# Kernel optimization log

Hardware: AMD Instinct MI355X
Metric: run time of the kernel (lower is better)

The kernel has to match this reference:

```python
import jax, jax.numpy as jnp
from jax import lax
import numpy as np

B, C_IN, C_OUT, H, W = 4, 256, 256, 4, 8192
HD = C_OUT // H          # head_dim = 64
K_ATT = 7
PAD = (1 * (K_ATT - 1) + 1) // 2  # = 3 (dilation=1)
CK = 1                   # conv_kernel_size (must be 1 for the module's shapes to be consistent)


def setup_inputs() -> dict:
    key = jax.random.key(0)
    ks = jax.random.split(key, 14)
    s = 0.05
    inp = {
        "x": jax.random.normal(ks[0], (B, C_IN, W), dtype=jnp.float32),
        # 1x1 convs q/k/v: weight [C_out, C_in], bias [C_out]
        "w1": jax.random.normal(ks[1], (C_OUT, C_IN), dtype=jnp.float32) * (C_IN ** -0.5),
        "b1": jax.random.normal(ks[2], (C_OUT,), dtype=jnp.float32) * s,
        "w2": jax.random.normal(ks[3], (C_OUT, C_IN), dtype=jnp.float32) * (C_IN ** -0.5),
        "b2": jax.random.normal(ks[4], (C_OUT,), dtype=jnp.float32) * s,
        "w3": jax.random.normal(ks[5], (C_OUT, C_IN), dtype=jnp.float32) * (C_IN ** -0.5),
        "b3": jax.random.normal(ks[6], (C_OUT,), dtype=jnp.float32) * s,
        # conv_p: Conv1d(1, head_dim, 1): weight [HD], bias [HD]
        "wp": jax.random.normal(ks[7], (HD,), dtype=jnp.float32) * s,
        "bp": jax.random.normal(ks[8], (HD,), dtype=jnp.float32) * s,
        # fc: Conv2d(3*H, CK, 1, bias=False): weight [CK, 3H]
        "fc_w": jax.random.normal(ks[9], (CK, 3 * H), dtype=jnp.float32) * ((3 * H) ** -0.5),
        # dep_conv: Conv1d(CK*HD -> C_OUT, kernel=CK, groups=HD): weight [C_OUT, CK, CK], bias [C_OUT]
        "dep_w": jax.random.normal(ks[10], (C_OUT, CK, CK), dtype=jnp.float32) * s,
        "dep_b": jax.random.normal(ks[11], (C_OUT,), dtype=jnp.float32) * s,
        "rate1": jnp.float32(0.5),
        "rate2": jnp.float32(0.5),
    }
    return inp


def _conv1x1(x, w, b):  # x: [B, Cin, W] -> [B, Cout, W]
    return jnp.einsum('oc,bcw->bow', w, x) + b[None, :, None]


def _unfold(p):  # p: [..., Wp] -> windows [..., W, K_ATT]
    idx = jnp.arange(W)[:, None] + jnp.arange(K_ATT)[None, :]
    return p[..., idx]


def _forward(x, w1, b1, w2, b2, w3, b3, wp, bp, fc_w, dep_w, dep_b, rate1, rate2):
    q = _conv1x1(x, w1, b1)   # [B, C, W]
    k = _conv1x1(x, w2, b2)
    v = _conv1x1(x, w3, b3)
    scaling = HD ** -0.5

    # positional encoding: conv_p(linspace(-1,1,W)) -> [HD, W]
    loc = jnp.linspace(-1.0, 1.0, W, dtype=jnp.float32)
    pe = wp[:, None] * loc[None, :] + bp[:, None]

    q_att = q.reshape(B * H, HD, W) * scaling
    k_att = k.reshape(B * H, HD, W)
    v_att = v.reshape(B * H, HD, W)

    # reflection pad last axis by PAD, then unfold to [.., HD, W, K]
    pad3 = lambda t: jnp.pad(t, ((0, 0), (0, 0), (PAD, PAD)), mode='reflect')
    uk = _unfold(pad3(k_att))                                   # [BH, HD, W, K]
    uv = _unfold(pad3(v_att))                                   # [BH, HD, W, K]
    upe = _unfold(jnp.pad(pe, ((0, 0), (PAD, PAD)), mode='reflect'))  # [HD, W, K]

    # att = sum_d q * (unfold_k + q_pe - unfold_rpe); softmax over window K
    D = pe[:, :, None] - upe                                     # [HD, W, K]
    att = jnp.einsum('bdw,bdwk->bwk', q_att, uk + D[None])       # [BH, W, K]
    att = jax.nn.softmax(att, axis=-1)
    out_att = jnp.einsum('bwk,bdwk->bdw', att, uv).reshape(B, C_OUT, W)

    # conv branch: fc over concatenated heads, then grouped dep_conv
    qkv = jnp.concatenate([q.reshape(B, H, HD, W),
                           k.reshape(B, H, HD, W),
                           v.reshape(B, H, HD, W)], axis=1)      # [B, 3H, HD, W]
    f_all = jnp.einsum('oc,bcdw->bodw', fc_w, qkv)               # [B, CK, HD, W]
    f_conv = jnp.transpose(f_all, (0, 2, 1, 3)).reshape(B, HD * CK, W)
    out_conv = lax.conv_general_dilated(
        f_conv, dep_w, window_strides=(1,), padding='VALID',
        dimension_numbers=('NCH', 'OIH', 'NCH'), feature_group_count=HD)
    out_conv = out_conv + dep_b[None, :, None]

    return rate1 * out_att + rate2 * out_conv


def reference(x, w1, b1, w2, b2, w3, b3, wp, bp, fc_w, dep_w, dep_b, rate1, rate2):
    return _forward(x, w1, b1, w2, b2, w3, b3, wp, bp, fc_w, dep_w, dep_b, rate1, rate2)
```

## Files before the change

kernel.cpp:

```cpp
#include <hip/hip_runtime.h>
#include <stdint.h>
#include <stddef.h>

typedef unsigned short u16;
typedef unsigned int   u32;

typedef __attribute__((ext_vector_type(8))) short bf16x8;
typedef __attribute__((ext_vector_type(4))) float f32x4;

__device__ __forceinline__ float b2f(u16 u)    { return __uint_as_float(((u32)u) << 16); }
__device__ __forceinline__ float b2f_lo(u32 v) { return __uint_as_float(v << 16); }
__device__ __forceinline__ float b2f_hi(u32 v) { return __uint_as_float(v & 0xFFFF0000u); }
__device__ __forceinline__ u16 f2b(float f){
  u32 x = __float_as_uint(f);
  return (u16)((x + 0x7FFFu + ((x >> 16) & 1u)) >> 16);
}

__global__ __launch_bounds__(256) void k_transpose(const float* __restrict__ x, u16* __restrict__ xt){
  __shared__ u16 tile[64 * 65];
  const int wt = blockIdx.x, ct = blockIdx.y, b = blockIdx.z;
  const int W0 = wt << 6, C0 = ct << 6;
  const int t = threadIdx.x;
#pragma unroll
  for (int it = 0; it < 4; ++it){
    const int task = t + (it << 8);
    const int c = task >> 4, u = task & 15;
    const float4 d = *(const float4*)(x + ((size_t)((b << 8) + C0 + c) << 13) + W0 + (u << 2));
    const int base = c * 65 + (u << 2);
    tile[base + 0] = f2b(d.x); tile[base + 1] = f2b(d.y);
    tile[base + 2] = f2b(d.z); tile[base + 3] = f2b(d.w);
  }
  __syncthreads();
#pragma unroll
  for (int it = 0; it < 2; ++it){
    const int task = t + (it << 8);
    const int wr = task >> 3, cu = task & 7;
    const int cb = cu << 3;
    u32 a0 = (u32)tile[(cb + 0) * 65 + wr] | ((u32)tile[(cb + 1) * 65 + wr] << 16);
    u32 a1 = (u32)tile[(cb + 2) * 65 + wr] | ((u32)tile[(cb + 3) * 65 + wr] << 16);
    u32 a2 = (u32)tile[(cb + 4) * 65 + wr] | ((u32)tile[(cb + 5) * 65 + wr] << 16);
    u32 a3 = (u32)tile[(cb + 6) * 65 + wr] | ((u32)tile[(cb + 7) * 65 + wr] << 16);
    uint4 val = make_uint4(a0, a1, a2, a3);
    *(uint4*)(xt + ((size_t)((b << 13) + W0 + wr) << 8) + C0 + cb) = val;
  }
}

__global__ __launch_bounds__(256) void k_build(const float* __restrict__ w1, const float* __restrict__ b1,
                                               const float* __restrict__ w2, const float* __restrict__ b2,
                                               const float* __restrict__ w3, const float* __restrict__ b3,
                                               const float* __restrict__ fcw,
                                               u16* __restrict__ Wall, float* __restrict__ ball){
  const int r = blockIdx.x, c = threadIdx.x;
  float v = 0.f, bv = 0.f;
  if (r < 256){      v = w1[(r << 8) + c];          bv = b1[r]; }
  else if (r < 512){ v = w2[((r - 256) << 8) + c];  bv = b2[r - 256]; }
  else if (r < 768){ v = w3[((r - 512) << 8) + c];  bv = b3[r - 512]; }
  else if (r < 832){
    const int d = r - 768;
    float s = 0.f, sbias = 0.f;
#pragma unroll
    for (int h = 0; h < 4; ++h){
      const int ch = (h << 6) + d;
      const float f1 = fcw[h], f2 = fcw[4 + h], f3 = fcw[8 + h];
      s     += f1 * w1[(ch << 8) + c] + f2 * w2[(ch << 8) + c] + f3 * w3[(ch << 8) + c];
      sbias += f1 * b1[ch] + f2 * b2[ch] + f3 * b3[ch];
    }
    v = s; bv = sbias;
  }
  Wall[(r << 8) + c] = f2b(v);
  if (c == 0) ball[r] = bv;
}

__global__ __launch_bounds__(256) void gemm_qkv(const u16* __restrict__ Wall, const float* __restrict__ ball,
                                                const u16* __restrict__ xt, u16* __restrict__ qkvt){
  __shared__ __align__(16) u16 As[128 * 64];
  __shared__ __align__(16) u16 Bs[128 * 64];
  const int mt = blockIdx.x, nt = blockIdx.y;
  const int b = nt >> 6;
  const int w0 = (nt & 63) << 7;
  const int tid = threadIdx.x;
  const int wave = tid >> 6, lane = tid & 63;
  const int wy = wave >> 1, wx = wave & 1;
  const int m0 = mt << 7;
  const int quad = lane >> 4, l15 = lane & 15;
  f32x4 acc[4][4] = {};

  for (int kc = 0; kc < 256; kc += 64){
    uint4 ra[4], rb[4];
#pragma unroll
    for (int k = 0; k < 4; ++k){
      const int cid = tid + (k << 8);
      const int row = cid >> 3, u = cid & 7;
      ra[k] = *(const uint4*)(Wall + ((m0 + row) << 8) + kc + (u << 3));
      rb[k] = *(const uint4*)(xt + (((size_t)((b << 13) + w0 + row)) << 8) + kc + (u << 3));
    }
    __syncthreads();
#pragma unroll
    for (int k = 0; k < 4; ++k){
      const int cid = tid + (k << 8);
      const int row = cid >> 3, u = cid & 7;
      *(uint4*)(As + (row << 6) + (u << 3)) = ra[k];
      *(uint4*)(Bs + (row << 6) + (u << 3)) = rb[k];
    }
    __syncthreads();
#pragma unroll
    for (int ks = 0; ks < 2; ++ks){
      bf16x8 av[4], bvv[4];
#pragma unroll
      for (int i = 0; i < 4; ++i){
        const int rowA = (wy << 6) + (i << 4) + l15;
        av[i] = *(const bf16x8*)(As + (rowA << 6) + (((ks << 2) + quad) << 3));
        const int rowB = (wx << 6) + (i << 4) + l15;
        bvv[i] = *(const bf16x8*)(Bs + (rowB << 6) + (((ks << 2) + quad) << 3));
      }
#pragma unroll
      for (int i = 0; i < 4; ++i)
#pragma unroll
        for (int j = 0; j < 4; ++j)
          acc[i][j] = __builtin_amdgcn_mfma_f32_16x16x32_bf16(av[i], bvv[j], acc[i][j], 0, 0, 0);
    }
  }

#pragma unroll
  for (int i = 0; i < 4; ++i){
    const int m = m0 + (wy << 6) + (i << 4) + (quad << 2);
    if (m < 832){
      const float4 bias = *(const float4*)(ball + m);
#pragma unroll
      for (int j = 0; j < 4; ++j){
        const int w = w0 + (wx << 6) + (j << 4) + l15;
        f32x4 r = acc[i][j];
        u32 lo = (u32)f2b(r.x + bias.x) | ((u32)f2b(r.y + bias.y) << 16);
        u32 hi = (u32)f2b(r.z + bias.z) | ((u32)f2b(r.w + bias.w) << 16);
        uint2 val; val.x = lo; val.y = hi;
        *(uint2*)(qkvt + ((size_t)((b << 13) + w)) * 832 + m) = val;
      }
    }
  }
}

__global__ __launch_bounds__(256) void attn_out(const u16* __restrict__ qkvt, const float* __restrict__ wp,
                                                const float* __restrict__ depw, const float* __restrict__ depb,
                                                const float* __restrict__ r1p, const float* __restrict__ r2p,
                                                float* __restrict__ out){
  __shared__ __align__(16) u16 sb[262 * 32];
  __shared__ float wpL[64];
  const int wt = blockIdx.x, h = blockIdx.y, b = blockIdx.z;
  const int w0 = wt << 8;
  const int t = threadIdx.x;
  const int w = w0 + t;
  if (t < 64) wpL[t] = wp[t];

  const u16* rowp = qkvt + ((size_t)((b << 13) + w)) * 832;
  uint4 qreg[8];
#pragma unroll
  for (int j = 0; j < 8; ++j) qreg[j] = *(const uint4*)(rowp + (h << 6) + (j << 3));
  float fv[16];
  {
    uint4 f0 = *(const uint4*)(rowp + 768 + (h << 4));
    uint4 f1 = *(const uint4*)(rowp + 768 + (h << 4) + 8);
    fv[0] = b2f_lo(f0.x); fv[1] = b2f_hi(f0.x); fv[2]  = b2f_lo(f0.y); fv[3]  = b2f_hi(f0.y);
    fv[4] = b2f_lo(f0.z); fv[5] = b2f_hi(f0.z); fv[6]  = b2f_lo(f0.w); fv[7]  = b2f_hi(f0.w);
    fv[8] = b2f_lo(f1.x); fv[9] = b2f_hi(f1.x); fv[10] = b2f_lo(f1.y); fv[11] = b2f_hi(f1.y);
    fv[12]= b2f_lo(f1.z); fv[13]= b2f_hi(f1.z); fv[14] = b2f_lo(f1.w); fv[15] = b2f_hi(f1.w);
  }

  float att[7] = {0.f,0.f,0.f,0.f,0.f,0.f,0.f};
  float qd = 0.f;

#pragma unroll
  for (int half = 0; half < 2; ++half){
    __syncthreads();
    for (int idx = t; idx < 262 * 4; idx += 256){
      const int row = idx >> 2, u = idx & 3;
      int wsrc = w0 - 3 + row;
      wsrc = wsrc < 0 ? -wsrc : (wsrc > 8191 ? 16382 - wsrc : wsrc);
      const uint4 d = *(const uint4*)(qkvt + ((size_t)((b << 13) + wsrc)) * 832 + 256 + (h << 6) + (half << 5) + (u << 3));
      *(uint4*)(sb + (row << 5) + (((u + (row >> 1)) & 3) << 3)) = d;
    }
    __syncthreads();
#pragma unroll
    for (int jj = 0; jj < 4; ++jj){
      const int j = (half << 2) + jj;
      float qf[8];
      {
        const uint4 q4 = qreg[j];
        qf[0] = b2f_lo(q4.x); qf[1] = b2f_hi(q4.x); qf[2] = b2f_lo(q4.y); qf[3] = b2f_hi(q4.y);
        qf[4] = b2f_lo(q4.z); qf[5] = b2f_hi(q4.z); qf[6] = b2f_lo(q4.w); qf[7] = b2f_hi(q4.w);
      }
#pragma unroll
      for (int e = 0; e < 8; ++e) qd += qf[e] * wpL[(j << 3) + e];
#pragma unroll
      for (int kk = 0; kk < 7; ++kk){
        const int r = t + kk;
        const uint4 kv = *(const uint4*)(sb + (r << 5) + (((jj + (r >> 1)) & 3) << 3));
        float a = att[kk];
        a += qf[0] * b2f_lo(kv.x) + qf[1] * b2f_hi(kv.x) + qf[2] * b2f_lo(kv.y) + qf[3] * b2f_hi(kv.y)
           + qf[4] * b2f_lo(kv.z) + qf[5] * b2f_hi(kv.z) + qf[6] * b2f_lo(kv.w) + qf[7] * b2f_hi(kv.w);
        att[kk] = a;
      }
    }
  }

  const float locw = -1.f + (2.f / 8191.f) * (float)w;
  float mx = -1e30f;
#pragma unroll
  for (int kk = 0; kk < 7; ++kk){
    int wr = w + kk - 3;
    wr = wr < 0 ? -wr : (wr > 8191 ? 16382 - wr : wr);
    const float lr = -1.f + (2.f / 8191.f) * (float)wr;
    att[kk] = 0.125f * (att[kk] + (locw - lr) * qd);
    mx = fmaxf(mx, att[kk]);
  }
  float p[7]; float ssum = 0.f;
#pragma unroll
  for (int kk = 0; kk < 7; ++kk){ p[kk] = __expf(att[kk] - mx); ssum += p[kk]; }
  const float inv = 1.f / ssum;
#pragma unroll
  for (int kk = 0; kk < 7; ++kk) p[kk] *= inv;

  const float r1 = r1p[0];
  const float r2 = r2p[0];

#pragma unroll
  for (int half = 0; half < 2; ++half){
    __syncthreads();
    for (int idx = t; idx < 262 * 4; idx += 256){
      const int row = idx >> 2, u = idx & 3;
      int wsrc = w0 - 3 + row;
      wsrc = wsrc < 0 ? -wsrc : (wsrc > 8191 ? 16382 - wsrc : wsrc);
      const uint4 d = *(const uint4*)(qkvt + ((size_t)((b << 13) + wsrc)) * 832 + 512 + (h << 6) + (half << 5) + (u << 3));
      *(uint4*)(sb + (row << 5) + (((u + (row >> 1)) & 3) << 3)) = d;
    }
    __syncthreads();
#pragma unroll
    for (int jj = 0; jj < 4; ++jj){
      float o[8] = {0.f,0.f,0.f,0.f,0.f,0.f,0.f,0.f};
#pragma unroll
      for (int kk = 0; kk < 7; ++kk){
        const int r = t + kk;
        const uint4 vv = *(const uint4*)(sb + (r << 5) + (((jj + (r >> 1)) & 3) << 3));
        const float pk = p[kk];
        o[0] += pk * b2f_lo(vv.x); o[1] += pk * b2f_hi(vv.x);
        o[2] += pk * b2f_lo(vv.y); o[3] += pk * b2f_hi(vv.y);
        o[4] += pk * b2f_lo(vv.z); o[5] += pk * b2f_hi(vv.z);
        o[6] += pk * b2f_lo(vv.w); o[7] += pk * b2f_hi(vv.w);
      }
      const int dl0 = (half << 5) + (jj << 3);
#pragma unroll
      for (int e = 0; e < 8; ++e){
        const int dl = dl0 + e;
        const float oc = depw[(h << 6) + dl] * fv[dl >> 2] + depb[(h << 6) + dl];
        out[(((size_t)((b << 8) + (h << 6) + dl)) << 13) + w] = r1 * o[e] + r2 * oc;
      }
    }
  }
}

extern "C" void kernel_launch(void* const* d_in, const int* in_sizes, int n_in,
                              void* d_out, int out_size, void* d_ws, size_t ws_size,
                              hipStream_t stream){
  (void)in_sizes; (void)n_in; (void)out_size; (void)ws_size;
  const float* x    = (const float*)d_in[0];
  const float* w1   = (const float*)d_in[1];
  const float* b1   = (const float*)d_in[2];
  const float* w2   = (const float*)d_in[3];
  const float* b2   = (const float*)d_in[4];
  const float* w3   = (const float*)d_in[5];
  const float* b3   = (const float*)d_in[6];
  const float* wp   = (const float*)d_in[7];
  const float* fcw  = (const float*)d_in[9];
  const float* depw = (const float*)d_in[10];
  const float* depb = (const float*)d_in[11];
  const float* r1p  = (const float*)d_in[12];
  const float* r2p  = (const float*)d_in[13];
  float* out = (float*)d_out;

  char* ws = (char*)d_ws;
  u16*   xt   = (u16*)(ws);
  u16*   Wall = (u16*)(ws + 16777216);
  float* ball = (float*)(ws + 17235968);
  u16*   qkvt = (u16*)(ws + 17239552);

  k_transpose<<<dim3(128, 4, 4), 256, 0, stream>>>(x, xt);
  k_build<<<dim3(896, 1, 1), 256, 0, stream>>>(w1, b1, w2, b2, w3, b3, fcw, Wall, ball);
  gemm_qkv<<<dim3(7, 256, 1), 256, 0, stream>>>(Wall, ball, xt, qkvt);
  attn_out<<<dim3(32, 4, 4), 256, 0, stream>>>(qkvt, wp, depw, depb, r1p, r2p, out);
}
```

Before: 231.7 us.

## Store qkv intermediate channel-major and stage per-wave K/V windows in shared memory

```diff
diff --git a/kernel.cpp b/kernel.cpp
--- a/kernel.cpp
+++ b/kernel.cpp
@@ -9,8 +9,6 @@
 typedef __attribute__((ext_vector_type(4))) float f32x4;
 
 __device__ __forceinline__ float b2f(u16 u)    { return __uint_as_float(((u32)u) << 16); }
-__device__ __forceinline__ float b2f_lo(u32 v) { return __uint_as_float(v << 16); }
-__device__ __forceinline__ float b2f_hi(u32 v) { return __uint_as_float(v & 0xFFFF0000u); }
 __device__ __forceinline__ u16 f2b(float f){
   u32 x = __float_as_uint(f);
   return (u16)((x + 0x7FFFu + ((x >> 16) & 1u)) >> 16);
@@ -123,17 +121,18 @@
 
 #pragma unroll
   for (int i = 0; i < 4; ++i){
-    const int m = m0 + (wy << 6) + (i << 4) + (quad << 2);
-    if (m < 832){
-      const float4 bias = *(const float4*)(ball + m);
+    const int mB = m0 + (wy << 6) + (i << 4) + (quad << 2);
+    if (mB < 832){
+      const float4 bias = *(const float4*)(ball + mB);
 #pragma unroll
       for (int j = 0; j < 4; ++j){
         const int w = w0 + (wx << 6) + (j << 4) + l15;
-        f32x4 r = acc[i][j];
-        u32 lo = (u32)f2b(r.x + bias.x) | ((u32)f2b(r.y + bias.y) << 16);
-        u32 hi = (u32)f2b(r.z + bias.z) | ((u32)f2b(r.w + bias.w) << 16);
-        uint2 val; val.x = lo; val.y = hi;
-        *(uint2*)(qkvt + ((size_t)((b << 13) + w)) * 832 + m) = val;
+        const f32x4 rr = acc[i][j];
+        const size_t base = (((size_t)(b * 832 + mB)) << 13) + w;
+        qkvt[base        ] = f2b(rr.x + bias.x);
+        qkvt[base +  8192] = f2b(rr.y + bias.y);
+        qkvt[base + 16384] = f2b(rr.z + bias.z);
+        qkvt[base + 24576] = f2b(rr.w + bias.w);
       }
     }
   }
@@ -143,62 +142,48 @@
                                                 const float* __restrict__ depw, const float* __restrict__ depb,
                                                 const float* __restrict__ r1p, const float* __restrict__ r2p,
                                                 float* __restrict__ out){
-  __shared__ __align__(16) u16 sb[262 * 32];
-  __shared__ float wpL[64];
+  __shared__ u16 kbuf[4][8][72];
   const int wt = blockIdx.x, h = blockIdx.y, b = blockIdx.z;
-  const int w0 = wt << 8;
   const int t = threadIdx.x;
-  const int w = w0 + t;
-  if (t < 64) wpL[t] = wp[t];
-
-  const u16* rowp = qkvt + ((size_t)((b << 13) + w)) * 832;
-  uint4 qreg[8];
-#pragma unroll
-  for (int j = 0; j < 8; ++j) qreg[j] = *(const uint4*)(rowp + (h << 6) + (j << 3));
-  float fv[16];
-  {
-    uint4 f0 = *(const uint4*)(rowp + 768 + (h << 4));
-    uint4 f1 = *(const uint4*)(rowp + 768 + (h << 4) + 8);
-    fv[0] = b2f_lo(f0.x); fv[1] = b2f_hi(f0.x); fv[2]  = b2f_lo(f0.y); fv[3]  = b2f_hi(f0.y);
-    fv[4] = b2f_lo(f0.z); fv[5] = b2f_hi(f0.z); fv[6]  = b2f_lo(f0.w); fv[7]  = b2f_hi(f0.w);
-    fv[8] = b2f_lo(f1.x); fv[9] = b2f_hi(f1.x); fv[10] = b2f_lo(f1.y); fv[11] = b2f_hi(f1.y);
-    fv[12]= b2f_lo(f1.z); fv[13]= b2f_hi(f1.z); fv[14] = b2f_lo(f1.w); fv[15] = b2f_hi(f1.w);
-  }
+  const int wave = t >> 6, lane = t & 63;
+  const int wbase = (wt << 8) + (wave << 6);
+  const int w = wbase + lane;
+
+  const size_t qbase = ((size_t)(b * 832 + (h << 6))) << 13;
+  const size_t kbase = ((size_t)(b * 832 + 256 + (h << 6))) << 13;
+  const size_t vbase = ((size_t)(b * 832 + 512 + (h << 6))) << 13;
+  const size_t fbase = ((size_t)(b * 832 + 768 + (h << 4))) << 13;
 
   float att[7] = {0.f,0.f,0.f,0.f,0.f,0.f,0.f};
   float qd = 0.f;
 
-#pragma unroll
-  for (int half = 0; half < 2; ++half){
-    __syncthreads();
-    for (int idx = t; idx < 262 * 4; idx += 256){
-      const int row = idx >> 2, u = idx & 3;
-      int wsrc = w0 - 3 + row;
-      wsrc = wsrc < 0 ? -wsrc : (wsrc > 8191 ? 16382 - wsrc : wsrc);
-      const uint4 d = *(const uint4*)(qkvt + ((size_t)((b << 13) + wsrc)) * 832 + 256 + (h << 6) + (half << 5) + (u << 3));
-      *(uint4*)(sb + (row << 5) + (((u + (row >> 1)) & 3) << 3)) = d;
-    }
-    __syncthreads();
-#pragma unroll
-    for (int jj = 0; jj < 4; ++jj){
-      const int j = (half << 2) + jj;
-      float qf[8];
-      {
-        const uint4 q4 = qreg[j];
-        qf[0] = b2f_lo(q4.x); qf[1] = b2f_hi(q4.x); qf[2] = b2f_lo(q4.y); qf[3] = b2f_hi(q4.y);
-        qf[4] = b2f_lo(q4.z); qf[5] = b2f_hi(q4.z); qf[6] = b2f_lo(q4.w); qf[7] = b2f_hi(q4.w);
-      }
-#pragma unroll
-      for (int e = 0; e < 8; ++e) qd += qf[e] * wpL[(j << 3) + e];
-#pragma unroll
-      for (int kk = 0; kk < 7; ++kk){
-        const int r = t + kk;
-        const uint4 kv = *(const uint4*)(sb + (r << 5) + (((jj + (r >> 1)) & 3) << 3));
-        float a = att[kk];
-        a += qf[0] * b2f_lo(kv.x) + qf[1] * b2f_hi(kv.x) + qf[2] * b2f_lo(kv.y) + qf[3] * b2f_hi(kv.y)
-           + qf[4] * b2f_lo(kv.z) + qf[5] * b2f_hi(kv.z) + qf[6] * b2f_lo(kv.w) + qf[7] * b2f_hi(kv.w);
-        att[kk] = a;
-      }
+  for (int bb = 0; bb < 8; ++bb){
+    __syncthreads();
+#pragma unroll
+    for (int r = 0; r < 8; ++r){
+      const int d = (bb << 3) + r;
+      const u16* krow = qkvt + kbase + ((size_t)d << 13);
+      int ws1 = wbase - 3 + lane;
+      ws1 = ws1 < 0 ? -ws1 : ws1;
+      kbuf[wave][r][lane] = krow[ws1];
+      if (lane < 6){
+        int ws2 = wbase + 61 + lane;
+        ws2 = ws2 > 8191 ? 16382 - ws2 : ws2;
+        kbuf[wave][r][64 + lane] = krow[ws2];
+      }
+    }
+    float qv[8];
+#pragma unroll
+    for (int r = 0; r < 8; ++r)
+      qv[r] = b2f(qkvt[qbase + ((size_t)((bb << 3) + r) << 13) + w]);
+    __syncthreads();
+#pragma unroll
+    for (int r = 0; r < 8; ++r){
+      const int d = (bb << 3) + r;
+      qd += qv[r] * wp[d];
+#pragma unroll
+      for (int kk = 0; kk < 7; ++kk)
+        att[kk] += qv[r] * b2f(kbuf[wave][r][lane + kk]);
     }
   }
 
@@ -222,37 +207,35 @@
   const float r1 = r1p[0];
   const float r2 = r2p[0];
 
-#pragma unroll
-  for (int half = 0; half < 2; ++half){
-    __syncthreads();
-    for (int idx = t; idx < 262 * 4; idx += 256){
-      const int row = idx >> 2, u = idx & 3;
-      int wsrc = w0 - 3 + row;
-      wsrc = wsrc < 0 ? -wsrc : (wsrc > 8191 ? 16382 - wsrc : wsrc);
-      const uint4 d = *(const uint4*)(qkvt + ((size_t)((b << 13) + wsrc)) * 832 + 512 + (h << 6) + (half << 5) + (u << 3));
-      *(uint4*)(sb + (row << 5) + (((u + (row >> 1)) & 3) << 3)) = d;
-    }
-    __syncthreads();
-#pragma unroll
-    for (int jj = 0; jj < 4; ++jj){
-      float o[8] = {0.f,0.f,0.f,0.f,0.f,0.f,0.f,0.f};
-#pragma unroll
-      for (int kk = 0; kk < 7; ++kk){
-        const int r = t + kk;
-        const uint4 vv = *(const uint4*)(sb + (r << 5) + (((jj + (r >> 1)) & 3) << 3));
-        const float pk = p[kk];
-        o[0] += pk * b2f_lo(vv.x); o[1] += pk * b2f_hi(vv.x);
-        o[2] += pk * b2f_lo(vv.y); o[3] += pk * b2f_hi(vv.y);
-        o[4] += pk * b2f_lo(vv.z); o[5] += pk * b2f_hi(vv.z);
-        o[6] += pk * b2f_lo(vv.w); o[7] += pk * b2f_hi(vv.w);
-      }
-      const int dl0 = (half << 5) + (jj << 3);
-#pragma unroll
-      for (int e = 0; e < 8; ++e){
-        const int dl = dl0 + e;
-        const float oc = depw[(h << 6) + dl] * fv[dl >> 2] + depb[(h << 6) + dl];
-        out[(((size_t)((b << 8) + (h << 6) + dl)) << 13) + w] = r1 * o[e] + r2 * oc;
-      }
+  for (int bb = 0; bb < 8; ++bb){
+    __syncthreads();
+#pragma unroll
+    for (int r = 0; r < 8; ++r){
+      const int d = (bb << 3) + r;
+      const u16* vrow = qkvt + vbase + ((size_t)d << 13);
+      int ws1 = wbase - 3 + lane;
+      ws1 = ws1 < 0 ? -ws1 : ws1;
+      kbuf[wave][r][lane] = vrow[ws1];
+      if (lane < 6){
+        int ws2 = wbase + 61 + lane;
+        ws2 = ws2 > 8191 ? 16382 - ws2 : ws2;
+        kbuf[wave][r][64 + lane] = vrow[ws2];
+      }
+    }
+    float fvv[2];
+#pragma unroll
+    for (int u = 0; u < 2; ++u)
+      fvv[u] = b2f(qkvt[fbase + ((size_t)((bb << 1) + u) << 13) + w]);
+    __syncthreads();
+#pragma unroll
+    for (int r = 0; r < 8; ++r){
+      const int d = (bb << 3) + r;
+      float o = 0.f;
+#pragma unroll
+      for (int kk = 0; kk < 7; ++kk)
+        o += p[kk] * b2f(kbuf[wave][r][lane + kk]);
+      const float oc = depw[(h << 6) + d] * fvv[r >> 2] + depb[(h << 6) + d];
+      out[(((size_t)((b << 8) + (h << 6) + d)) << 13) + w] = r1 * o + r2 * oc;
     }
   }
 }
```

Result: slower. 282.6 us (+22.0%).
